# Optimization experiments

Measured on AMD Instinct MI355X. Metric: run time of the kernel, lower is better.

The kernel has to match this reference:

```python
import jax, jax.numpy as jnp
import numpy as np

NEG_INF = -1.0e9  # matches masked_fill value in the torch module


def setup_inputs() -> dict:
    key = jax.random.key(0)
    ks = jax.random.split(key, 6)
    B, N, H, D, A = 64, 2048, 512, 512, 512
    h = jax.random.normal(ks[0], (B, H), dtype=jnp.float32)
    enc_mem = jax.random.normal(ks[1], (B, N, D), dtype=jnp.float32)
    enc_mask = jax.random.randint(ks[2], (B, N), 0, 2, dtype=jnp.int32)
    # nn.Linear weights are (out_features, in_features); scale like default init
    W_h = jax.random.normal(ks[3], (A, H), dtype=jnp.float32) / np.sqrt(H)
    W_e = jax.random.normal(ks[4], (A, D), dtype=jnp.float32) / np.sqrt(D)
    v = jax.random.normal(ks[5], (A,), dtype=jnp.float32) / np.sqrt(A)
    return {"h": h, "enc_mem": enc_mem, "enc_mask": enc_mask,
            "W_h": W_h, "W_e": W_e, "v": v}


def reference(h, enc_mem, enc_mask, W_h, W_e, v):
    # energy: (B, N, A) = tanh(W_h h [broadcast over N] + W_e enc_mem)
    proj_h = jnp.einsum('bh,ah->ba', h, W_h)            # (B, A)
    proj_e = jnp.einsum('bnd,ad->bna', enc_mem, W_e)    # (B, N, A)
    energy = jnp.tanh(proj_h[:, None, :] + proj_e)      # (B, N, A)
    scores = jnp.einsum('bna,a->bn', energy, v)         # (B, N)
    scores = jnp.where(enc_mask == 0, NEG_INF, scores)
    alpha = jax.nn.softmax(scores, axis=-1)             # (B, N)
    context = jnp.einsum('bn,bnd->bd', alpha, enc_mem)  # (B, D)
    return (context, alpha)
```

## Files before the change

### kernel.cpp

```cpp
#include <hip/hip_runtime.h>
#include <hip/hip_bf16.h>
#include <cstdint>
#include <cstddef>

#define NEG_INF (-1.0e9f)

typedef __attribute__((ext_vector_type(8))) short bf16x8;
typedef __attribute__((ext_vector_type(4))) float f32x4;

constexpr int BB = 64;
constexpr int NN = 2048;
constexpr int HH = 512;
constexpr int DD = 512;
constexpr int AA = 512;

__device__ __forceinline__ float fast_rcp(float x) {
#if __has_builtin(__builtin_amdgcn_rcpf)
  return __builtin_amdgcn_rcpf(x);
#else
  return 1.f / x;
#endif
}

__device__ __forceinline__ float fast_tanh(float x) {
  float e = __expf(2.f * fabsf(x));
  float t = 1.f - 2.f * fast_rcp(e + 1.f);
  return copysignf(t, x);
}

__device__ __forceinline__ bf16x8 pack8(const float4& lo, const float4& hi) {
  __hip_bfloat162 a = __float22bfloat162_rn(float2{lo.x, lo.y});
  __hip_bfloat162 b = __float22bfloat162_rn(float2{lo.z, lo.w});
  __hip_bfloat162 c = __float22bfloat162_rn(float2{hi.x, hi.y});
  __hip_bfloat162 d = __float22bfloat162_rn(float2{hi.z, hi.w});
  union { unsigned int w[4]; bf16x8 v; } u;
  __builtin_memcpy(&u.w[0], &a, 4);
  __builtin_memcpy(&u.w[1], &b, 4);
  __builtin_memcpy(&u.w[2], &c, 4);
  __builtin_memcpy(&u.w[3], &d, 4);
  return u.v;
}

__global__ __launch_bounds__(256)
void we_cast_kernel(const float* __restrict__ We, unsigned short* __restrict__ web) {
  const int gid  = blockIdx.x * 256 + threadIdx.x;
  const int l    = gid & 63;
  const int tile = gid >> 6;
  const int jc   = tile >> 4;
  const int kg   = tile & 15;
  const float* src = We + (size_t)(jc * 16 + (l & 15)) * DD + kg * 32 + (l >> 4) * 8;
  float4 s0 = *(const float4*)src;
  float4 s1 = *(const float4*)(src + 4);
  *(bf16x8*)(web + (size_t)tile * 512 + l * 8) = pack8(s0, s1);
}

__global__ __launch_bounds__(256)
void proj_h_kernel(const float* __restrict__ h, const float* __restrict__ Wh,
                   float* __restrict__ ph) {
  __shared__ float hL[HH];
  const int b = blockIdx.x;
  hL[threadIdx.x]       = h[b * HH + threadIdx.x];
  hL[threadIdx.x + 256] = h[b * HH + threadIdx.x + 256];
  __syncthreads();
  const int a = blockIdx.y * 256 + threadIdx.x;
  const float4* wr = (const float4*)(Wh + (size_t)a * HH);
  float acc = 0.f;
  #pragma unroll 4
  for (int j = 0; j < HH / 4; ++j) {
    float4 w = wr[j];
    acc += w.x * hL[4*j] + w.y * hL[4*j+1] + w.z * hL[4*j+2] + w.w * hL[4*j+3];
  }
  ph[b * AA + a] = acc;
}

__global__ __launch_bounds__(512, 2)
void scores_fullk(const float* __restrict__ enc, const unsigned short* __restrict__ web,
                  const float* __restrict__ ph, const float* __restrict__ vvec,
                  float* __restrict__ scores) {
  constexpr int RR  = 128;
  constexpr int CK  = 128;
  constexpr int LDK = 136;

  __shared__ unsigned short As[2][RR * LDK];
  __shared__ float sred[4][RR];

  const int tid  = threadIdx.x;
  const int lane = tid & 63;
  const int wid  = tid >> 6;
  const int wr   = wid >> 2;
  const int wc   = wid & 3;
  const int c    = lane & 15;
  const int quad = lane >> 4;

  const int r0 = blockIdx.x * RR;
  const int b  = r0 >> 11;

  const int srow = (tid * 8) >> 7;
  const int scol = (tid * 8) & 127;
  const float* encBase = enc + (size_t)r0 * DD;

  float4 lo[4], hi[4];

  auto LOADREGS = [&](int kc) {
    #pragma unroll
    for (int s = 0; s < 4; ++s) {
      const float* p = encBase + (size_t)(srow + s * 32) * DD + kc * CK + scol;
      lo[s] = *(const float4*)p;
      hi[s] = *(const float4*)(p + 4);
    }
  };
  auto WRITE = [&](int buf) {
    #pragma unroll
    for (int s = 0; s < 4; ++s)
      *(bf16x8*)&As[buf][(srow + s * 32) * LDK + scol] = pack8(lo[s], hi[s]);
  };

  const unsigned short* bTile = web + (size_t)(wc * 8) * 16 * 512 + (lane << 3);

  float pp[8], vv[8];
  #pragma unroll
  for (int j = 0; j < 8; ++j) {
    const int col = wc * 128 + j * 16 + c;
    pp[j] = ph[b * AA + col];
    vv[j] = vvec[col];
  }

  f32x4 acc[4][8];
  #pragma unroll
  for (int i = 0; i < 4; ++i)
    #pragma unroll
    for (int j = 0; j < 8; ++j)
      acc[i][j] = (f32x4){0.f, 0.f, 0.f, 0.f};

  LOADREGS(0);
  WRITE(0);
  __syncthreads();

  #pragma unroll
  for (int kc = 0; kc < 4; ++kc) {
    const int cur = kc & 1;
    if (kc < 3) LOADREGS(kc + 1);

    const unsigned short* aB = &As[cur][(wr * 64 + c) * LDK + quad * 8];
    const int kg0 = kc * (CK / 32);
    #pragma unroll
    for (int k0 = 0; k0 < CK; k0 += 32) {
      const int kg = kg0 + (k0 >> 5);
      bf16x8 bfr[8];
      #pragma unroll
      for (int j = 0; j < 8; ++j)
        bfr[j] = *(const bf16x8*)(bTile + ((size_t)(j * 16 + kg) << 9));
      bf16x8 af[4];
      #pragma unroll
      for (int i = 0; i < 4; ++i)
        af[i] = *(const bf16x8*)(aB + i * 16 * LDK + k0);
      #pragma unroll
      for (int i = 0; i < 4; ++i)
        #pragma unroll
        for (int j = 0; j < 8; ++j)
          acc[i][j] = __builtin_amdgcn_mfma_f32_16x16x32_bf16(af[i], bfr[j], acc[i][j], 0, 0, 0);
    }

    if (kc < 3) WRITE(cur ^ 1);
    __syncthreads();
  }

  #pragma unroll
  for (int i = 0; i < 4; ++i) {
    #pragma unroll
    for (int r = 0; r < 4; ++r) {
      float p = 0.f;
      #pragma unroll
      for (int j = 0; j < 8; ++j)
        p += vv[j] * fast_tanh(acc[i][j][r] + pp[j]);
      p += __shfl_xor(p, 1, 64);
      p += __shfl_xor(p, 2, 64);
      p += __shfl_xor(p, 4, 64);
      p += __shfl_xor(p, 8, 64);
      if (c == 0) sred[wc][wr * 64 + i * 16 + quad * 4 + r] = p;
    }
  }
  __syncthreads();
  if (tid < RR)
    scores[r0 + tid] = sred[0][tid] + sred[1][tid] + sred[2][tid] + sred[3][tid];
}

__global__ __launch_bounds__(256)
void softmax_kernel(const float* __restrict__ scores, const int* __restrict__ mask,
                    float* __restrict__ alpha) {
  const int b = blockIdx.x, tid = threadIdx.x;
  const int base = b * NN;
  float vals[8];
  float mx = -3.4e38f;
  #pragma unroll
  for (int i = 0; i < 8; ++i) {
    int n = tid + 256 * i;
    float s = scores[base + n];
    if (mask[base + n] == 0) s = NEG_INF;
    vals[i] = s;
    mx = fmaxf(mx, s);
  }
  #pragma unroll
  for (int o = 32; o; o >>= 1) mx = fmaxf(mx, __shfl_xor(mx, o, 64));
  __shared__ float w4[4];
  if ((tid & 63) == 0) w4[tid >> 6] = mx;
  __syncthreads();
  mx = fmaxf(fmaxf(w4[0], w4[1]), fmaxf(w4[2], w4[3]));
  float sum = 0.f;
  #pragma unroll
  for (int i = 0; i < 8; ++i) { vals[i] = __expf(vals[i] - mx); sum += vals[i]; }
  #pragma unroll
  for (int o = 32; o; o >>= 1) sum += __shfl_xor(sum, o, 64);
  __shared__ float s4[4];
  if ((tid & 63) == 0) s4[tid >> 6] = sum;
  __syncthreads();
  sum = s4[0] + s4[1] + s4[2] + s4[3];
  float inv = 1.f / sum;
  #pragma unroll
  for (int i = 0; i < 8; ++i) alpha[base + tid + 256 * i] = vals[i] * inv;
}

__global__ __launch_bounds__(128)
void context_part(const float* __restrict__ enc, const float* __restrict__ alpha,
                  float* __restrict__ cpart) {
  const int b  = blockIdx.x;
  const int nc = blockIdx.y;
  const int t  = threadIdx.x;
  __shared__ float aL[64];
  if (t < 64) aL[t] = alpha[b * NN + nc * 64 + t];
  __syncthreads();
  const float* ep = enc + ((size_t)b * NN + nc * 64) * DD + t * 4;
  float4 a0 = {0.f, 0.f, 0.f, 0.f}, a1 = {0.f, 0.f, 0.f, 0.f};
  float4 a2 = {0.f, 0.f, 0.f, 0.f}, a3 = {0.f, 0.f, 0.f, 0.f};
  #pragma unroll 4
  for (int n = 0; n < 64; n += 4) {
    float4 e0 = *(const float4*)(ep + (size_t)n * DD);
    float4 e1 = *(const float4*)(ep + (size_t)(n + 1) * DD);
    float4 e2 = *(const float4*)(ep + (size_t)(n + 2) * DD);
    float4 e3 = *(const float4*)(ep + (size_t)(n + 3) * DD);
    float s0 = aL[n], s1 = aL[n + 1], s2 = aL[n + 2], s3 = aL[n + 3];
    a0.x += s0 * e0.x; a0.y += s0 * e0.y; a0.z += s0 * e0.z; a0.w += s0 * e0.w;
    a1.x += s1 * e1.x; a1.y += s1 * e1.y; a1.z += s1 * e1.z; a1.w += s1 * e1.w;
    a2.x += s2 * e2.x; a2.y += s2 * e2.y; a2.z += s2 * e2.z; a2.w += s2 * e2.w;
    a3.x += s3 * e3.x; a3.y += s3 * e3.y; a3.z += s3 * e3.z; a3.w += s3 * e3.w;
  }
  a0.x += a1.x + a2.x + a3.x;
  a0.y += a1.y + a2.y + a3.y;
  a0.z += a1.z + a2.z + a3.z;
  a0.w += a1.w + a2.w + a3.w;
  *(float4*)(cpart + ((size_t)(b * 32 + nc)) * DD + t * 4) = a0;
}

__global__ __launch_bounds__(256)
void context_reduce(const float* __restrict__ cpart, float* __restrict__ ctx) {
  const int i = blockIdx.x * 256 + threadIdx.x;
  const int b = i >> 9, d = i & 511;
  float s = 0.f;
  #pragma unroll
  for (int nc = 0; nc < 32; ++nc) s += cpart[((size_t)(b * 32 + nc)) * DD + d];
  ctx[i] = s;
}

extern "C" void kernel_launch(void* const* d_in, const int* in_sizes, int n_in,
                              void* d_out, int out_size, void* d_ws, size_t ws_size,
                              hipStream_t stream) {
  const float* h    = (const float*)d_in[0];
  const float* enc  = (const float*)d_in[1];
  const int*   mask = (const int*)d_in[2];
  const float* Wh   = (const float*)d_in[3];
  const float* We   = (const float*)d_in[4];
  const float* v    = (const float*)d_in[5];

  float* out   = (float*)d_out;
  float* ctx   = out;
  float* alpha = out + BB * DD;

  char* w = (char*)d_ws;
  unsigned short* web = (unsigned short*)w;
  float* ph     = (float*)(w + (size_t)AA * DD * 2);
  float* scores = ph + BB * AA;
  float* cpart  = scores + BB * NN;

  we_cast_kernel<<<(AA * DD / 8) / 256, 256, 0, stream>>>(We, web);
  proj_h_kernel<<<dim3(BB, 2), 256, 0, stream>>>(h, Wh, ph);
  scores_fullk<<<(BB * NN) / 128, 512, 0, stream>>>(enc, web, ph, v, scores);
  softmax_kernel<<<BB, 256, 0, stream>>>(scores, mask, alpha);
  context_part<<<dim3(BB, 32), 128, 0, stream>>>(enc, alpha, cpart);
  context_reduce<<<(BB * DD) / 256, 256, 0, stream>>>(cpart, ctx);
  (void)in_sizes; (void)n_in; (void)out_size; (void)ws_size;
}
```

Baseline: 490.8 us.

## Fuse context accumulation into scores kernel with online-softmax partials

The scores kernel now keeps the whole bf16 tile of encoder rows in shared memory. After computing scores it does a block-local masked softmax and accumulates a partial weighted context from that resident tile, emitting per-block max and sum. A small combine kernel rescales and merges the partials. This removes the second global read of enc_mem and the old context_part/context_reduce kernels. In exchange, shared memory per block grows, which can lower occupancy, and the context is now computed from bf16-rounded encoder values.

```diff
diff --git a/kernel.cpp b/kernel.cpp
--- a/kernel.cpp
+++ b/kernel.cpp
@@ -26,6 +26,10 @@
   float e = __expf(2.f * fabsf(x));
   float t = 1.f - 2.f * fast_rcp(e + 1.f);
   return copysignf(t, x);
+}
+
+__device__ __forceinline__ float bf2f(unsigned short u) {
+  return __uint_as_float(((unsigned int)u) << 16);
 }
 
 __device__ __forceinline__ bf16x8 pack8(const float4& lo, const float4& hi) {
@@ -74,15 +78,20 @@
 }
 
 __global__ __launch_bounds__(512, 2)
-void scores_fullk(const float* __restrict__ enc, const unsigned short* __restrict__ web,
-                  const float* __restrict__ ph, const float* __restrict__ vvec,
-                  float* __restrict__ scores) {
+void scores_ctx_fused(const float* __restrict__ enc, const unsigned short* __restrict__ web,
+                      const float* __restrict__ ph, const float* __restrict__ vvec,
+                      const int* __restrict__ mask,
+                      float* __restrict__ scores, float* __restrict__ cpart,
+                      float* __restrict__ ml) {
   constexpr int RR  = 128;
   constexpr int CK  = 128;
-  constexpr int LDK = 136;
-
-  __shared__ unsigned short As[2][RR * LDK];
+  constexpr int LDA = 520;
+
+  __shared__ unsigned short As[RR * LDA];
   __shared__ float sred[4][RR];
+  __shared__ float sfin[RR];
+  __shared__ float wgt[RR];
+  __shared__ float mlred[2];
 
   const int tid  = threadIdx.x;
   const int lane = tid & 63;
@@ -94,6 +103,7 @@
 
   const int r0 = blockIdx.x * RR;
   const int b  = r0 >> 11;
+  const int blk = blockIdx.x & 15;
 
   const int srow = (tid * 8) >> 7;
   const int scol = (tid * 8) & 127;
@@ -109,10 +119,10 @@
       hi[s] = *(const float4*)(p + 4);
     }
   };
-  auto WRITE = [&](int buf) {
+  auto WRITE = [&](int kc) {
     #pragma unroll
     for (int s = 0; s < 4; ++s)
-      *(bf16x8*)&As[buf][(srow + s * 32) * LDK + scol] = pack8(lo[s], hi[s]);
+      *(bf16x8*)&As[(srow + s * 32) * LDA + kc * CK + scol] = pack8(lo[s], hi[s]);
   };
 
   const unsigned short* bTile = web + (size_t)(wc * 8) * 16 * 512 + (lane << 3);
@@ -138,10 +148,9 @@
 
   #pragma unroll
   for (int kc = 0; kc < 4; ++kc) {
-    const int cur = kc & 1;
     if (kc < 3) LOADREGS(kc + 1);
 
-    const unsigned short* aB = &As[cur][(wr * 64 + c) * LDK + quad * 8];
+    const unsigned short* aB = &As[(wr * 64 + c) * LDA + kc * CK + quad * 8];
     const int kg0 = kc * (CK / 32);
     #pragma unroll
     for (int k0 = 0; k0 < CK; k0 += 32) {
@@ -153,7 +162,7 @@
       bf16x8 af[4];
       #pragma unroll
       for (int i = 0; i < 4; ++i)
-        af[i] = *(const bf16x8*)(aB + i * 16 * LDK + k0);
+        af[i] = *(const bf16x8*)(aB + i * 16 * LDA + k0);
       #pragma unroll
       for (int i = 0; i < 4; ++i)
         #pragma unroll
@@ -161,7 +170,7 @@
           acc[i][j] = __builtin_amdgcn_mfma_f32_16x16x32_bf16(af[i], bfr[j], acc[i][j], 0, 0, 0);
     }
 
-    if (kc < 3) WRITE(cur ^ 1);
+    if (kc < 3) WRITE(kc + 1);
     __syncthreads();
   }
 
@@ -181,8 +190,50 @@
     }
   }
   __syncthreads();
-  if (tid < RR)
-    scores[r0 + tid] = sred[0][tid] + sred[1][tid] + sred[2][tid] + sred[3][tid];
+
+  if (tid < RR) {
+    float s = sred[0][tid] + sred[1][tid] + sred[2][tid] + sred[3][tid];
+    scores[r0 + tid] = s;
+    sfin[tid] = (mask[r0 + tid] == 0) ? NEG_INF : s;
+  }
+  __syncthreads();
+
+  if (tid < 64) {
+    float v = fmaxf(sfin[tid], sfin[tid + 64]);
+    #pragma unroll
+    for (int o = 32; o; o >>= 1) v = fmaxf(v, __shfl_xor(v, o, 64));
+    if (tid == 0) mlred[0] = v;
+  }
+  __syncthreads();
+  const float mblk = mlred[0];
+
+  if (tid < 64) {
+    float w0 = __expf(sfin[tid] - mblk);
+    float w1 = __expf(sfin[tid + 64] - mblk);
+    wgt[tid] = w0; wgt[tid + 64] = w1;
+    float v = w0 + w1;
+    #pragma unroll
+    for (int o = 32; o; o >>= 1) v += __shfl_xor(v, o, 64);
+    if (tid == 0) mlred[1] = v;
+  }
+  __syncthreads();
+
+  {
+    const unsigned short* colp = &As[tid];
+    float a0 = 0.f, a1 = 0.f, a2 = 0.f, a3 = 0.f;
+    #pragma unroll 4
+    for (int r = 0; r < RR; r += 4) {
+      a0 += wgt[r]     * bf2f(colp[(size_t)(r    ) * LDA]);
+      a1 += wgt[r + 1] * bf2f(colp[(size_t)(r + 1) * LDA]);
+      a2 += wgt[r + 2] * bf2f(colp[(size_t)(r + 2) * LDA]);
+      a3 += wgt[r + 3] * bf2f(colp[(size_t)(r + 3) * LDA]);
+    }
+    cpart[((size_t)(b * 16 + blk)) * DD + tid] = (a0 + a1) + (a2 + a3);
+  }
+  if (tid == 0) {
+    ml[(b * 16 + blk) * 2]     = mblk;
+    ml[(b * 16 + blk) * 2 + 1] = mlred[1];
+  }
 }
 
 __global__ __launch_bounds__(256)
@@ -220,45 +271,28 @@
   for (int i = 0; i < 8; ++i) alpha[base + tid + 256 * i] = vals[i] * inv;
 }
 
-__global__ __launch_bounds__(128)
-void context_part(const float* __restrict__ enc, const float* __restrict__ alpha,
-                  float* __restrict__ cpart) {
-  const int b  = blockIdx.x;
-  const int nc = blockIdx.y;
-  const int t  = threadIdx.x;
-  __shared__ float aL[64];
-  if (t < 64) aL[t] = alpha[b * NN + nc * 64 + t];
-  __syncthreads();
-  const float* ep = enc + ((size_t)b * NN + nc * 64) * DD + t * 4;
-  float4 a0 = {0.f, 0.f, 0.f, 0.f}, a1 = {0.f, 0.f, 0.f, 0.f};
-  float4 a2 = {0.f, 0.f, 0.f, 0.f}, a3 = {0.f, 0.f, 0.f, 0.f};
-  #pragma unroll 4
-  for (int n = 0; n < 64; n += 4) {
-    float4 e0 = *(const float4*)(ep + (size_t)n * DD);
-    float4 e1 = *(const float4*)(ep + (size_t)(n + 1) * DD);
-    float4 e2 = *(const float4*)(ep + (size_t)(n + 2) * DD);
-    float4 e3 = *(const float4*)(ep + (size_t)(n + 3) * DD);
-    float s0 = aL[n], s1 = aL[n + 1], s2 = aL[n + 2], s3 = aL[n + 3];
-    a0.x += s0 * e0.x; a0.y += s0 * e0.y; a0.z += s0 * e0.z; a0.w += s0 * e0.w;
-    a1.x += s1 * e1.x; a1.y += s1 * e1.y; a1.z += s1 * e1.z; a1.w += s1 * e1.w;
-    a2.x += s2 * e2.x; a2.y += s2 * e2.y; a2.z += s2 * e2.z; a2.w += s2 * e2.w;
-    a3.x += s3 * e3.x; a3.y += s3 * e3.y; a3.z += s3 * e3.z; a3.w += s3 * e3.w;
-  }
-  a0.x += a1.x + a2.x + a3.x;
-  a0.y += a1.y + a2.y + a3.y;
-  a0.z += a1.z + a2.z + a3.z;
-  a0.w += a1.w + a2.w + a3.w;
-  *(float4*)(cpart + ((size_t)(b * 32 + nc)) * DD + t * 4) = a0;
-}
-
-__global__ __launch_bounds__(256)
-void context_reduce(const float* __restrict__ cpart, float* __restrict__ ctx) {
-  const int i = blockIdx.x * 256 + threadIdx.x;
-  const int b = i >> 9, d = i & 511;
-  float s = 0.f;
-  #pragma unroll
-  for (int nc = 0; nc < 32; ++nc) s += cpart[((size_t)(b * 32 + nc)) * DD + d];
-  ctx[i] = s;
+__global__ __launch_bounds__(512)
+void context_combine(const float* __restrict__ cpart, const float* __restrict__ ml,
+                     float* __restrict__ ctx) {
+  const int b = blockIdx.x, t = threadIdx.x;
+  __shared__ float mls[32];
+  if (t < 32) mls[t] = ml[b * 32 + t];
+  __syncthreads();
+  float M = -3.4e38f;
+  #pragma unroll
+  for (int i = 0; i < 16; ++i) M = fmaxf(M, mls[2 * i]);
+  float w[16];
+  float L = 0.f;
+  #pragma unroll
+  for (int i = 0; i < 16; ++i) {
+    w[i] = __expf(mls[2 * i] - M);
+    L += mls[2 * i + 1] * w[i];
+  }
+  float acc = 0.f;
+  #pragma unroll
+  for (int i = 0; i < 16; ++i)
+    acc += w[i] * cpart[((size_t)(b * 16 + i)) * DD + t];
+  ctx[b * DD + t] = acc / L;
 }
 
 extern "C" void kernel_launch(void* const* d_in, const int* in_sizes, int n_in,
@@ -280,12 +314,13 @@
   float* ph     = (float*)(w + (size_t)AA * DD * 2);
   float* scores = ph + BB * AA;
   float* cpart  = scores + BB * NN;
+  float* ml     = cpart + BB * 16 * DD;
 
   we_cast_kernel<<<(AA * DD / 8) / 256, 256, 0, stream>>>(We, web);
   proj_h_kernel<<<dim3(BB, 2), 256, 0, stream>>>(h, Wh, ph);
-  scores_fullk<<<(BB * NN) / 128, 512, 0, stream>>>(enc, web, ph, v, scores);
+  scores_ctx_fused<<<(BB * NN) / 128, 512, 0, stream>>>(enc, web, ph, v, mask,
+                                                        scores, cpart, ml);
   softmax_kernel<<<BB, 256, 0, stream>>>(scores, mask, alpha);
-  context_part<<<dim3(BB, 32), 128, 0, stream>>>(enc, alpha, cpart);
-  context_reduce<<<(BB * DD) / 256, 256, 0, stream>>>(cpart, ctx);
+  context_combine<<<BB, 512, 0, stream>>>(cpart, ml, ctx);
   (void)in_sizes; (void)n_in; (void)out_size; (void)ws_size;
 }
```

New measurement: 468.9 us. -4.4%, faster.
